# Performance work log

Hardware: AMD Instinct MI355X
Metric: run time of the kernel (lower is better)

## Reference

```python
import jax, jax.numpy as jnp
import numpy as np

N, C_IN, H, W = 64, 8, 256, 256
E = 4      # edge_emb_dim
D = 4      # node_emb_dim
K = 3      # kernel_size
DN = ('NCHW', 'OIHW', 'NCHW')


def conv2d(x, w, b, padding):
    y = jax.lax.conv_general_dilated(x, w, (1, 1), padding, dimension_numbers=DN)
    return y + b[None, :, None, None]


def _w(key, shape):
    fan_in = shape[1] * shape[2] * shape[3]
    return jax.random.normal(key, shape, dtype=jnp.float32) / np.sqrt(fan_in)


def setup_inputs() -> dict:
    key = jax.random.key(0)
    ks = jax.random.split(key, 16)
    return {
        'x': jax.random.normal(ks[0], (N, C_IN, H, W), dtype=jnp.float32),
        # downsampling: 1x1 conv C_IN -> E (kernel=stride=downsampling_factor=1)
        'w_down': _w(ks[1], (E, C_IN, 1, 1)), 'b_down': jnp.zeros((E,), jnp.float32),
        # edge network phi: two conv3x3 (E->E) each followed by silu
        'w_e1': _w(ks[2], (E, E, K, K)), 'b_e1': jnp.zeros((E,), jnp.float32),
        'w_e2': _w(ks[3], (E, E, K, K)), 'b_e2': jnp.zeros((E,), jnp.float32),
        # upsampling: ConvTranspose with kernel=stride=1 == 1x1 conv E -> E
        'w_up': _w(ks[4], (E, E, 1, 1)), 'b_up': jnp.zeros((E,), jnp.float32),
        # node network psi: conv3x3 (C_IN+E -> D), silu, conv3x3 (D -> D)
        'w_n1': _w(ks[5], (D, C_IN + E, K, K)), 'b_n1': jnp.zeros((D,), jnp.float32),
        'w_n2': _w(ks[6], (D, D, K, K)), 'b_n2': jnp.zeros((D,), jnp.float32),
        # pre_resid: 1x1 conv C_IN -> D (since in_channels != node_emb_dim)
        'w_r': _w(ks[7], (D, C_IN, 1, 1)), 'b_r': jnp.zeros((D,), jnp.float32),
    }


def reference(x, w_down, b_down, w_e1, b_e1, w_e2, b_e2, w_up, b_up,
              w_n1, b_n1, w_n2, b_n2, w_r, b_r):
    # vmap(downsampling)(x): treat cell axis N as conv batch. (N,E,H,W)
    z = conv2d(x, w_down, b_down, 'VALID')
    # cell-wise edge CNN phi
    h = jax.nn.silu(conv2d(z, w_e1, b_e1, 'SAME'))
    h = jax.nn.silu(conv2d(h, w_e2, b_e2, 'SAME'))
    # sum-aggregate over cells -> A: (E,H,W)
    A = h.sum(axis=0)
    # upsampling (kernel=stride=1 transpose conv == 1x1 conv); pad is a no-op here
    A = conv2d(A[None], w_up, b_up, 'VALID')[0]
    # node update: concat [x, A] on channels, cell-interaction CNN psi
    y = jnp.concatenate([x, jnp.broadcast_to(A[None], (N, E, H, W))], axis=1)
    y = jax.nn.silu(conv2d(y, w_n1, b_n1, 'SAME'))
    y = conv2d(y, w_n2, b_n2, 'SAME')
    # residual with channel-matching 1x1 conv
    y = y + conv2d(x, w_r, b_r, 'VALID')
    return y
```

## Files before the change

### kernel.cpp

```cpp
#include <hip/hip_runtime.h>
#include <hip/hip_bf16.h>

#define NCELL 64
#define CIN 8
#define EE 4
#define DD 4
#define HH 256
#define WW 256

#define TW 32
#define TH 16
#define ZW (TW + 4)
#define ZH (TH + 4)
#define HW1 (TW + 2)
#define HH1 (TH + 2)
#define NCG 4

__device__ __forceinline__ float silu(float v) {
    return v / (1.0f + __expf(-v));
}

__global__ __launch_bounds__(256) void zero_kernel(float* __restrict__ p) {
    int i = blockIdx.x * 256 + threadIdx.x;
    reinterpret_cast<float4*>(p)[i] = make_float4(0.f, 0.f, 0.f, 0.f);
}

__global__ __launch_bounds__(256) void edge_kernel(
    const float* __restrict__ x,
    const float* __restrict__ w_down, const float* __restrict__ b_down,
    const float* __restrict__ w_e1, const float* __restrict__ b_e1,
    const float* __restrict__ w_e2, const float* __restrict__ b_e2,
    float* __restrict__ A)
{
    __shared__ float zb[EE][ZH][ZW];
    __shared__ float h1b[EE][HH1][HW1];

    const int tid = threadIdx.x;
    const int ox = blockIdx.x * TW;
    const int oy = blockIdx.y * TH;
    const int n0 = blockIdx.z * NCG;

    float acc[2][EE];
#pragma unroll
    for (int k = 0; k < 2; ++k)
#pragma unroll
        for (int e = 0; e < EE; ++e) acc[k][e] = 0.f;

    for (int j = 0; j < NCG; ++j) {
        const int n = n0 + j;
        const float* __restrict__ xn = x + (size_t)n * CIN * HH * WW;

        for (int idx = tid; idx < ZH * ZW; idx += 256) {
            const int ly = idx / ZW, lx = idx % ZW;
            const int gy = oy + ly - 2, gx = ox + lx - 2;
            float zv[EE];
            if ((unsigned)gy < (unsigned)HH && (unsigned)gx < (unsigned)WW) {
                float xv[CIN];
#pragma unroll
                for (int c = 0; c < CIN; ++c)
                    xv[c] = xn[(c * HH + gy) * WW + gx];
#pragma unroll
                for (int e = 0; e < EE; ++e) {
                    float s = b_down[e];
#pragma unroll
                    for (int c = 0; c < CIN; ++c) s += xv[c] * w_down[e * CIN + c];
                    zv[e] = s;
                }
            } else {
#pragma unroll
                for (int e = 0; e < EE; ++e) zv[e] = 0.f;
            }
#pragma unroll
            for (int e = 0; e < EE; ++e) zb[e][ly][lx] = zv[e];
        }
        __syncthreads();

        for (int idx = tid; idx < HH1 * HW1; idx += 256) {
            const int ly = idx / HW1, lx = idx % HW1;
            const int gy = oy + ly - 1, gx = ox + lx - 1;
            float hv[EE];
            if ((unsigned)gy < (unsigned)HH && (unsigned)gx < (unsigned)WW) {
                float s[EE];
#pragma unroll
                for (int o = 0; o < EE; ++o) s[o] = b_e1[o];
#pragma unroll
                for (int i = 0; i < EE; ++i)
#pragma unroll
                    for (int dy = 0; dy < 3; ++dy)
#pragma unroll
                        for (int dx = 0; dx < 3; ++dx) {
                            const float a = zb[i][ly + dy][lx + dx];
#pragma unroll
                            for (int o = 0; o < EE; ++o)
                                s[o] += a * w_e1[o * 36 + i * 9 + dy * 3 + dx];
                        }
#pragma unroll
                for (int o = 0; o < EE; ++o) hv[o] = silu(s[o]);
            } else {
#pragma unroll
                for (int o = 0; o < EE; ++o) hv[o] = 0.f;
            }
#pragma unroll
            for (int o = 0; o < EE; ++o) h1b[o][ly][lx] = hv[o];
        }
        __syncthreads();

#pragma unroll
        for (int k = 0; k < 2; ++k) {
            const int idx = tid + k * 256;
            const int py = idx / TW, px = idx % TW;
            float s[EE];
#pragma unroll
            for (int o = 0; o < EE; ++o) s[o] = b_e2[o];
#pragma unroll
            for (int i = 0; i < EE; ++i)
#pragma unroll
                for (int dy = 0; dy < 3; ++dy)
#pragma unroll
                    for (int dx = 0; dx < 3; ++dx) {
                        const float a = h1b[i][py + dy][px + dx];
#pragma unroll
                        for (int o = 0; o < EE; ++o)
                            s[o] += a * w_e2[o * 36 + i * 9 + dy * 3 + dx];
                    }
#pragma unroll
            for (int o = 0; o < EE; ++o) acc[k][o] += silu(s[o]);
        }
        __syncthreads();
    }

#pragma unroll
    for (int k = 0; k < 2; ++k) {
        const int idx = tid + k * 256;
        const int py = idx / TW, px = idx % TW;
        const int gy = oy + py, gx = ox + px;
#pragma unroll
        for (int e = 0; e < EE; ++e)
            atomicAdd(&A[(e * HH + gy) * WW + gx], acc[k][e]);
    }
}

__global__ __launch_bounds__(256) void up_kernel(
    const float* __restrict__ A,
    const float* __restrict__ w_up, const float* __restrict__ b_up,
    float* __restrict__ Aup)
{
    const int p = blockIdx.x * 256 + threadIdx.x;
    float a[EE];
#pragma unroll
    for (int e = 0; e < EE; ++e) a[e] = A[e * (HH * WW) + p];
#pragma unroll
    for (int c = 0; c < EE; ++c) {
        float s = b_up[c];
#pragma unroll
        for (int e = 0; e < EE; ++e) s += a[e] * w_up[c * EE + e];
        Aup[c * (HH * WW) + p] = s;
    }
}

__global__ __launch_bounds__(256) void node_kernel(
    const float* __restrict__ x, const float* __restrict__ Aup,
    const float* __restrict__ w_n1, const float* __restrict__ b_n1,
    const float* __restrict__ w_n2, const float* __restrict__ b_n2,
    const float* __restrict__ w_r, const float* __restrict__ b_r,
    float* __restrict__ out)
{
    __shared__ float xa[CIN + EE][ZH][ZW];
    __shared__ float y1b[DD][HH1][HW1];

    const int tid = threadIdx.x;
    const int ox = blockIdx.x * TW;
    const int oy = blockIdx.y * TH;
    const int n = blockIdx.z;
    const float* __restrict__ xn = x + (size_t)n * CIN * HH * WW;

    for (int idx = tid; idx < ZH * ZW; idx += 256) {
        const int ly = idx / ZW, lx = idx % ZW;
        const int gy = oy + ly - 2, gx = ox + lx - 2;
        if ((unsigned)gy < (unsigned)HH && (unsigned)gx < (unsigned)WW) {
#pragma unroll
            for (int c = 0; c < CIN; ++c)
                xa[c][ly][lx] = xn[(c * HH + gy) * WW + gx];
#pragma unroll
            for (int e = 0; e < EE; ++e)
                xa[CIN + e][ly][lx] = Aup[(e * HH + gy) * WW + gx];
        } else {
#pragma unroll
            for (int c = 0; c < CIN + EE; ++c) xa[c][ly][lx] = 0.f;
        }
    }
    __syncthreads();

    for (int idx = tid; idx < HH1 * HW1; idx += 256) {
        const int ly = idx / HW1, lx = idx % HW1;
        const int gy = oy + ly - 1, gx = ox + lx - 1;
        float yv[DD];
        if ((unsigned)gy < (unsigned)HH && (unsigned)gx < (unsigned)WW) {
            float s[DD];
#pragma unroll
            for (int o = 0; o < DD; ++o) s[o] = b_n1[o];
#pragma unroll
            for (int i = 0; i < CIN + EE; ++i)
#pragma unroll
                for (int dy = 0; dy < 3; ++dy)
#pragma unroll
                    for (int dx = 0; dx < 3; ++dx) {
                        const float a = xa[i][ly + dy][lx + dx];
#pragma unroll
                        for (int o = 0; o < DD; ++o)
                            s[o] += a * w_n1[o * 108 + i * 9 + dy * 3 + dx];
                    }
#pragma unroll
            for (int o = 0; o < DD; ++o) yv[o] = silu(s[o]);
        } else {
#pragma unroll
            for (int o = 0; o < DD; ++o) yv[o] = 0.f;
        }
#pragma unroll
        for (int o = 0; o < DD; ++o) y1b[o][ly][lx] = yv[o];
    }
    __syncthreads();

#pragma unroll
    for (int k = 0; k < 2; ++k) {
        const int idx = tid + k * 256;
        const int py = idx / TW, px = idx % TW;
        const int gy = oy + py, gx = ox + px;
        float s[DD];
#pragma unroll
        for (int o = 0; o < DD; ++o) s[o] = b_n2[o] + b_r[o];
#pragma unroll
        for (int i = 0; i < DD; ++i)
#pragma unroll
            for (int dy = 0; dy < 3; ++dy)
#pragma unroll
                for (int dx = 0; dx < 3; ++dx) {
                    const float a = y1b[i][py + dy][px + dx];
#pragma unroll
                    for (int o = 0; o < DD; ++o)
                        s[o] += a * w_n2[o * 36 + i * 9 + dy * 3 + dx];
                }
#pragma unroll
        for (int c = 0; c < CIN; ++c) {
            const float xv = xa[c][py + 2][px + 2];
#pragma unroll
            for (int o = 0; o < DD; ++o) s[o] += xv * w_r[o * CIN + c];
        }
#pragma unroll
        for (int o = 0; o < DD; ++o)
            out[(((size_t)n * DD + o) * HH + gy) * WW + gx] = s[o];
    }
}

extern "C" void kernel_launch(void* const* d_in, const int* in_sizes, int n_in,
                              void* d_out, int out_size, void* d_ws, size_t ws_size,
                              hipStream_t stream) {
    const float* x      = (const float*)d_in[0];
    const float* w_down = (const float*)d_in[1];
    const float* b_down = (const float*)d_in[2];
    const float* w_e1   = (const float*)d_in[3];
    const float* b_e1   = (const float*)d_in[4];
    const float* w_e2   = (const float*)d_in[5];
    const float* b_e2   = (const float*)d_in[6];
    const float* w_up   = (const float*)d_in[7];
    const float* b_up   = (const float*)d_in[8];
    const float* w_n1   = (const float*)d_in[9];
    const float* b_n1   = (const float*)d_in[10];
    const float* w_n2   = (const float*)d_in[11];
    const float* b_n2   = (const float*)d_in[12];
    const float* w_r    = (const float*)d_in[13];
    const float* b_r    = (const float*)d_in[14];
    float* out = (float*)d_out;

    float* A   = (float*)d_ws;
    float* Aup = (float*)d_ws + EE * HH * WW;

    zero_kernel<<<dim3(256), dim3(256), 0, stream>>>(A);

    edge_kernel<<<dim3(WW / TW, HH / TH, NCELL / NCG), dim3(256), 0, stream>>>(
        x, w_down, b_down, w_e1, b_e1, w_e2, b_e2, A);

    up_kernel<<<dim3((HH * WW) / 256), dim3(256), 0, stream>>>(A, w_up, b_up, Aup);

    node_kernel<<<dim3(WW / TW, HH / TH, NCELL), dim3(256), 0, stream>>>(
        x, Aup, w_n1, b_n1, w_n2, b_n2, w_r, b_r, out);
}
```

Measured before the change: 296.3 us.

## Use channel-interleaved float4 smem, two-row register blocking, fuse upsample into node kernel

Shared-memory tiles switch from channel-planar float arrays to float4 per pixel, and A is stored pixel-interleaved so the node kernel can read it with one vector load. Each thread now computes two vertically adjacent output rows and reuses the overlapping input rows of the 3x3 window, which cuts LDS traffic per output. The separate up_kernel is removed and the 1x1 upsample is folded into the node kernel's tile load, dropping one launch and a full write and read of Aup. In exchange the node kernel recomputes the upsample for every cell and halo pixel, and register pressure per thread rises.

```diff
diff --git a/kernel.cpp b/kernel.cpp
--- a/kernel.cpp
+++ b/kernel.cpp
@@ -16,8 +16,46 @@
 #define HH1 (TH + 2)
 #define NCG 4
 
-__device__ __forceinline__ float silu(float v) {
-    return v / (1.0f + __expf(-v));
+#define COMP(v,i) ((i)==0?(v).x:(i)==1?(v).y:(i)==2?(v).z:(v).w)
+
+__device__ __forceinline__ void fma4(float4& a, float s, float4 w) {
+    a.x = fmaf(s, w.x, a.x);
+    a.y = fmaf(s, w.y, a.y);
+    a.z = fmaf(s, w.z, a.z);
+    a.w = fmaf(s, w.w, a.w);
+}
+
+__device__ __forceinline__ float4 ld4s(const float* __restrict__ p, int stride, int idx) {
+    return make_float4(p[idx], p[stride + idx], p[2 * stride + idx], p[3 * stride + idx]);
+}
+
+__device__ __forceinline__ float silu1(float v) { return v / (1.0f + __expf(-v)); }
+__device__ __forceinline__ float4 silu4(float4 v) {
+    return make_float4(silu1(v.x), silu1(v.y), silu1(v.z), silu1(v.w));
+}
+
+template<int LW>
+__device__ __forceinline__ void conv3x3_pair(const float4 (*in)[LW], int ly0, int lx,
+                                             const float* __restrict__ w, int wstride,
+                                             int ibase, float4& s0, float4& s1) {
+#pragma unroll
+    for (int dx = 0; dx < 3; ++dx) {
+        const float4 a0 = in[ly0 + 0][lx + dx];
+        const float4 a1 = in[ly0 + 1][lx + dx];
+        const float4 a2 = in[ly0 + 2][lx + dx];
+        const float4 a3 = in[ly0 + 3][lx + dx];
+#pragma unroll
+        for (int dy = 0; dy < 3; ++dy) {
+            const float4 va = (dy == 0) ? a0 : (dy == 1) ? a1 : a2;
+            const float4 vb = (dy == 0) ? a1 : (dy == 1) ? a2 : a3;
+#pragma unroll
+            for (int ci = 0; ci < 4; ++ci) {
+                const float4 w4 = ld4s(w, wstride, (ibase + ci) * 9 + dy * 3 + dx);
+                fma4(s0, COMP(va, ci), w4);
+                fma4(s1, COMP(vb, ci), w4);
+            }
+        }
+    }
 }
 
 __global__ __launch_bounds__(256) void zero_kernel(float* __restrict__ p) {
@@ -32,141 +70,90 @@
     const float* __restrict__ w_e2, const float* __restrict__ b_e2,
     float* __restrict__ A)
 {
-    __shared__ float zb[EE][ZH][ZW];
-    __shared__ float h1b[EE][HH1][HW1];
+    __shared__ float4 zb[ZH][ZW];
+    __shared__ float4 h1b[HH1][HW1];
 
     const int tid = threadIdx.x;
     const int ox = blockIdx.x * TW;
     const int oy = blockIdx.y * TH;
     const int n0 = blockIdx.z * NCG;
 
-    float acc[2][EE];
-#pragma unroll
-    for (int k = 0; k < 2; ++k)
-#pragma unroll
-        for (int e = 0; e < EE; ++e) acc[k][e] = 0.f;
+    const float4 be1 = make_float4(b_e1[0], b_e1[1], b_e1[2], b_e1[3]);
+    const float4 be2 = make_float4(b_e2[0], b_e2[1], b_e2[2], b_e2[3]);
+    const float4 bdn = make_float4(b_down[0], b_down[1], b_down[2], b_down[3]);
+
+    float4 acc0 = make_float4(0.f, 0.f, 0.f, 0.f);
+    float4 acc1 = make_float4(0.f, 0.f, 0.f, 0.f);
 
     for (int j = 0; j < NCG; ++j) {
         const int n = n0 + j;
         const float* __restrict__ xn = x + (size_t)n * CIN * HH * WW;
 
         for (int idx = tid; idx < ZH * ZW; idx += 256) {
-            const int ly = idx / ZW, lx = idx % ZW;
+            const int ly = idx / ZW, lx = idx - (idx / ZW) * ZW;
             const int gy = oy + ly - 2, gx = ox + lx - 2;
-            float zv[EE];
+            float4 zv = make_float4(0.f, 0.f, 0.f, 0.f);
             if ((unsigned)gy < (unsigned)HH && (unsigned)gx < (unsigned)WW) {
-                float xv[CIN];
-#pragma unroll
-                for (int c = 0; c < CIN; ++c)
-                    xv[c] = xn[(c * HH + gy) * WW + gx];
-#pragma unroll
-                for (int e = 0; e < EE; ++e) {
-                    float s = b_down[e];
-#pragma unroll
-                    for (int c = 0; c < CIN; ++c) s += xv[c] * w_down[e * CIN + c];
-                    zv[e] = s;
+                zv = bdn;
+#pragma unroll
+                for (int c = 0; c < CIN; ++c) {
+                    const float xv = xn[(c * HH + gy) * WW + gx];
+                    fma4(zv, xv, ld4s(w_down, CIN, c));
                 }
-            } else {
-#pragma unroll
-                for (int e = 0; e < EE; ++e) zv[e] = 0.f;
             }
-#pragma unroll
-            for (int e = 0; e < EE; ++e) zb[e][ly][lx] = zv[e];
+            zb[ly][lx] = zv;
         }
         __syncthreads();
 
-        for (int idx = tid; idx < HH1 * HW1; idx += 256) {
-            const int ly = idx / HW1, lx = idx % HW1;
-            const int gy = oy + ly - 1, gx = ox + lx - 1;
-            float hv[EE];
-            if ((unsigned)gy < (unsigned)HH && (unsigned)gx < (unsigned)WW) {
-                float s[EE];
-#pragma unroll
-                for (int o = 0; o < EE; ++o) s[o] = b_e1[o];
-#pragma unroll
-                for (int i = 0; i < EE; ++i)
-#pragma unroll
-                    for (int dy = 0; dy < 3; ++dy)
-#pragma unroll
-                        for (int dx = 0; dx < 3; ++dx) {
-                            const float a = zb[i][ly + dy][lx + dx];
-#pragma unroll
-                            for (int o = 0; o < EE; ++o)
-                                s[o] += a * w_e1[o * 36 + i * 9 + dy * 3 + dx];
-                        }
-#pragma unroll
-                for (int o = 0; o < EE; ++o) hv[o] = silu(s[o]);
-            } else {
-#pragma unroll
-                for (int o = 0; o < EE; ++o) hv[o] = 0.f;
-            }
-#pragma unroll
-            for (int o = 0; o < EE; ++o) h1b[o][ly][lx] = hv[o];
+        for (int t = tid; t < 9 * HW1; t += 256) {
+            const int pr = t / HW1;
+            const int lx = t - pr * HW1;
+            const int ly0 = pr * 2;
+            float4 s0 = be1, s1 = be1;
+            conv3x3_pair<ZW>(zb, ly0, lx, w_e1, 36, 0, s0, s1);
+            const int gx = ox + lx - 1;
+            const int gy0 = oy + ly0 - 1;
+            const bool xok = (unsigned)gx < (unsigned)WW;
+            h1b[ly0 + 0][lx] = (xok && (unsigned)(gy0 + 0) < (unsigned)HH)
+                                   ? silu4(s0) : make_float4(0.f, 0.f, 0.f, 0.f);
+            h1b[ly0 + 1][lx] = (xok && (unsigned)(gy0 + 1) < (unsigned)HH)
+                                   ? silu4(s1) : make_float4(0.f, 0.f, 0.f, 0.f);
         }
         __syncthreads();
 
-#pragma unroll
-        for (int k = 0; k < 2; ++k) {
-            const int idx = tid + k * 256;
-            const int py = idx / TW, px = idx % TW;
-            float s[EE];
-#pragma unroll
-            for (int o = 0; o < EE; ++o) s[o] = b_e2[o];
-#pragma unroll
-            for (int i = 0; i < EE; ++i)
-#pragma unroll
-                for (int dy = 0; dy < 3; ++dy)
-#pragma unroll
-                    for (int dx = 0; dx < 3; ++dx) {
-                        const float a = h1b[i][py + dy][px + dx];
-#pragma unroll
-                        for (int o = 0; o < EE; ++o)
-                            s[o] += a * w_e2[o * 36 + i * 9 + dy * 3 + dx];
-                    }
-#pragma unroll
-            for (int o = 0; o < EE; ++o) acc[k][o] += silu(s[o]);
+        {
+            const int py0 = (tid >> 5) * 2;
+            const int px = tid & 31;
+            float4 s0 = be2, s1 = be2;
+            conv3x3_pair<HW1>(h1b, py0, px, w_e2, 36, 0, s0, s1);
+            const float4 v0 = silu4(s0), v1 = silu4(s1);
+            acc0.x += v0.x; acc0.y += v0.y; acc0.z += v0.z; acc0.w += v0.w;
+            acc1.x += v1.x; acc1.y += v1.y; acc1.z += v1.z; acc1.w += v1.w;
         }
         __syncthreads();
     }
 
-#pragma unroll
-    for (int k = 0; k < 2; ++k) {
-        const int idx = tid + k * 256;
-        const int py = idx / TW, px = idx % TW;
-        const int gy = oy + py, gx = ox + px;
-#pragma unroll
-        for (int e = 0; e < EE; ++e)
-            atomicAdd(&A[(e * HH + gy) * WW + gx], acc[k][e]);
-    }
-}
-
-__global__ __launch_bounds__(256) void up_kernel(
-    const float* __restrict__ A,
+    const int py0 = (tid >> 5) * 2;
+    const int px = tid & 31;
+    const int gy0 = oy + py0, gx = ox + px;
+    float* a0 = &A[((size_t)(gy0 + 0) * WW + gx) * 4];
+    float* a1 = &A[((size_t)(gy0 + 1) * WW + gx) * 4];
+    atomicAdd(a0 + 0, acc0.x); atomicAdd(a0 + 1, acc0.y);
+    atomicAdd(a0 + 2, acc0.z); atomicAdd(a0 + 3, acc0.w);
+    atomicAdd(a1 + 0, acc1.x); atomicAdd(a1 + 1, acc1.y);
+    atomicAdd(a1 + 2, acc1.z); atomicAdd(a1 + 3, acc1.w);
+}
+
+__global__ __launch_bounds__(256) void node_kernel(
+    const float* __restrict__ x, const float* __restrict__ A,
     const float* __restrict__ w_up, const float* __restrict__ b_up,
-    float* __restrict__ Aup)
-{
-    const int p = blockIdx.x * 256 + threadIdx.x;
-    float a[EE];
-#pragma unroll
-    for (int e = 0; e < EE; ++e) a[e] = A[e * (HH * WW) + p];
-#pragma unroll
-    for (int c = 0; c < EE; ++c) {
-        float s = b_up[c];
-#pragma unroll
-        for (int e = 0; e < EE; ++e) s += a[e] * w_up[c * EE + e];
-        Aup[c * (HH * WW) + p] = s;
-    }
-}
-
-__global__ __launch_bounds__(256) void node_kernel(
-    const float* __restrict__ x, const float* __restrict__ Aup,
     const float* __restrict__ w_n1, const float* __restrict__ b_n1,
     const float* __restrict__ w_n2, const float* __restrict__ b_n2,
     const float* __restrict__ w_r, const float* __restrict__ b_r,
     float* __restrict__ out)
 {
-    __shared__ float xa[CIN + EE][ZH][ZW];
-    __shared__ float y1b[DD][HH1][HW1];
+    __shared__ float4 xa[3][ZH][ZW];
+    __shared__ float4 y1b[HH1][HW1];
 
     const int tid = threadIdx.x;
     const int ox = blockIdx.x * TW;
@@ -174,81 +161,72 @@
     const int n = blockIdx.z;
     const float* __restrict__ xn = x + (size_t)n * CIN * HH * WW;
 
+    const float4 bup = make_float4(b_up[0], b_up[1], b_up[2], b_up[3]);
+    const float4 bn1 = make_float4(b_n1[0], b_n1[1], b_n1[2], b_n1[3]);
+    const float4 bn2r = make_float4(b_n2[0] + b_r[0], b_n2[1] + b_r[1],
+                                    b_n2[2] + b_r[2], b_n2[3] + b_r[3]);
+
     for (int idx = tid; idx < ZH * ZW; idx += 256) {
-        const int ly = idx / ZW, lx = idx % ZW;
+        const int ly = idx / ZW, lx = idx - (idx / ZW) * ZW;
         const int gy = oy + ly - 2, gx = ox + lx - 2;
+        float4 g0 = make_float4(0.f, 0.f, 0.f, 0.f);
+        float4 g1 = g0, au = g0;
         if ((unsigned)gy < (unsigned)HH && (unsigned)gx < (unsigned)WW) {
-#pragma unroll
-            for (int c = 0; c < CIN; ++c)
-                xa[c][ly][lx] = xn[(c * HH + gy) * WW + gx];
-#pragma unroll
-            for (int e = 0; e < EE; ++e)
-                xa[CIN + e][ly][lx] = Aup[(e * HH + gy) * WW + gx];
-        } else {
-#pragma unroll
-            for (int c = 0; c < CIN + EE; ++c) xa[c][ly][lx] = 0.f;
-        }
+            g0 = make_float4(xn[(0 * HH + gy) * WW + gx], xn[(1 * HH + gy) * WW + gx],
+                             xn[(2 * HH + gy) * WW + gx], xn[(3 * HH + gy) * WW + gx]);
+            g1 = make_float4(xn[(4 * HH + gy) * WW + gx], xn[(5 * HH + gy) * WW + gx],
+                             xn[(6 * HH + gy) * WW + gx], xn[(7 * HH + gy) * WW + gx]);
+            const float4 a4 = reinterpret_cast<const float4*>(A)[gy * WW + gx];
+            au = bup;
+#pragma unroll
+            for (int e = 0; e < 4; ++e) fma4(au, COMP(a4, e), ld4s(w_up, EE, e));
+        }
+        xa[0][ly][lx] = g0;
+        xa[1][ly][lx] = g1;
+        xa[2][ly][lx] = au;
     }
     __syncthreads();
 
-    for (int idx = tid; idx < HH1 * HW1; idx += 256) {
-        const int ly = idx / HW1, lx = idx % HW1;
-        const int gy = oy + ly - 1, gx = ox + lx - 1;
-        float yv[DD];
-        if ((unsigned)gy < (unsigned)HH && (unsigned)gx < (unsigned)WW) {
-            float s[DD];
-#pragma unroll
-            for (int o = 0; o < DD; ++o) s[o] = b_n1[o];
-#pragma unroll
-            for (int i = 0; i < CIN + EE; ++i)
-#pragma unroll
-                for (int dy = 0; dy < 3; ++dy)
-#pragma unroll
-                    for (int dx = 0; dx < 3; ++dx) {
-                        const float a = xa[i][ly + dy][lx + dx];
-#pragma unroll
-                        for (int o = 0; o < DD; ++o)
-                            s[o] += a * w_n1[o * 108 + i * 9 + dy * 3 + dx];
-                    }
-#pragma unroll
-            for (int o = 0; o < DD; ++o) yv[o] = silu(s[o]);
-        } else {
-#pragma unroll
-            for (int o = 0; o < DD; ++o) yv[o] = 0.f;
-        }
-#pragma unroll
-        for (int o = 0; o < DD; ++o) y1b[o][ly][lx] = yv[o];
+    for (int t = tid; t < 9 * HW1; t += 256) {
+        const int pr = t / HW1;
+        const int lx = t - pr * HW1;
+        const int ly0 = pr * 2;
+        float4 s0 = bn1, s1 = bn1;
+#pragma unroll
+        for (int g = 0; g < 3; ++g)
+            conv3x3_pair<ZW>(xa[g], ly0, lx, w_n1, 108, g * 4, s0, s1);
+        const int gx = ox + lx - 1;
+        const int gy0 = oy + ly0 - 1;
+        const bool xok = (unsigned)gx < (unsigned)WW;
+        y1b[ly0 + 0][lx] = (xok && (unsigned)(gy0 + 0) < (unsigned)HH)
+                               ? silu4(s0) : make_float4(0.f, 0.f, 0.f, 0.f);
+        y1b[ly0 + 1][lx] = (xok && (unsigned)(gy0 + 1) < (unsigned)HH)
+                               ? silu4(s1) : make_float4(0.f, 0.f, 0.f, 0.f);
     }
     __syncthreads();
 
-#pragma unroll
-    for (int k = 0; k < 2; ++k) {
-        const int idx = tid + k * 256;
-        const int py = idx / TW, px = idx % TW;
-        const int gy = oy + py, gx = ox + px;
-        float s[DD];
-#pragma unroll
-        for (int o = 0; o < DD; ++o) s[o] = b_n2[o] + b_r[o];
-#pragma unroll
-        for (int i = 0; i < DD; ++i)
-#pragma unroll
-            for (int dy = 0; dy < 3; ++dy)
-#pragma unroll
-                for (int dx = 0; dx < 3; ++dx) {
-                    const float a = y1b[i][py + dy][px + dx];
-#pragma unroll
-                    for (int o = 0; o < DD; ++o)
-                        s[o] += a * w_n2[o * 36 + i * 9 + dy * 3 + dx];
-                }
-#pragma unroll
-        for (int c = 0; c < CIN; ++c) {
-            const float xv = xa[c][py + 2][px + 2];
-#pragma unroll
-            for (int o = 0; o < DD; ++o) s[o] += xv * w_r[o * CIN + c];
-        }
-#pragma unroll
-        for (int o = 0; o < DD; ++o)
-            out[(((size_t)n * DD + o) * HH + gy) * WW + gx] = s[o];
+    {
+        const int py0 = (tid >> 5) * 2;
+        const int px = tid & 31;
+        float4 s0 = bn2r, s1 = bn2r;
+        conv3x3_pair<HW1>(y1b, py0, px, w_n2, 36, 0, s0, s1);
+#pragma unroll
+        for (int g = 0; g < 2; ++g) {
+            const float4 c0 = xa[g][py0 + 2][px + 2];
+            const float4 c1 = xa[g][py0 + 3][px + 2];
+#pragma unroll
+            for (int ci = 0; ci < 4; ++ci) {
+                const float4 w4 = ld4s(w_r, CIN, g * 4 + ci);
+                fma4(s0, COMP(c0, ci), w4);
+                fma4(s1, COMP(c1, ci), w4);
+            }
+        }
+        const int gy0 = oy + py0, gx = ox + px;
+#pragma unroll
+        for (int o = 0; o < 4; ++o) {
+            out[(((size_t)n * DD + o) * HH + gy0 + 0) * WW + gx] = COMP(s0, o);
+            out[(((size_t)n * DD + o) * HH + gy0 + 1) * WW + gx] = COMP(s1, o);
+        }
     }
 }
 
@@ -272,16 +250,13 @@
     const float* b_r    = (const float*)d_in[14];
     float* out = (float*)d_out;
 
-    float* A   = (float*)d_ws;
-    float* Aup = (float*)d_ws + EE * HH * WW;
+    float* A = (float*)d_ws;
 
     zero_kernel<<<dim3(256), dim3(256), 0, stream>>>(A);
 
     edge_kernel<<<dim3(WW / TW, HH / TH, NCELL / NCG), dim3(256), 0, stream>>>(
         x, w_down, b_down, w_e1, b_e1, w_e2, b_e2, A);
 
-    up_kernel<<<dim3((HH * WW) / 256), dim3(256), 0, stream>>>(A, w_up, b_up, Aup);
-
     node_kernel<<<dim3(WW / TW, HH / TH, NCELL), dim3(256), 0, stream>>>(
-        x, Aup, w_n1, b_n1, w_n2, b_n2, w_r, b_r, out);
-}
+        x, A, w_up, b_up, w_n1, b_n1, w_n2, b_n2, w_r, b_r, out);
+}
```

Measured after the change: 402.2 us. 35.7% more time.
